# Performance work log

Hardware: AMD Instinct MI355X
Metric: run time of the kernel (lower is better)

## Reference

```python
import jax, jax.numpy as jnp
import numpy as np

EMBED_DIM = 1024
ZDIM = 128
STD = 0.02


def setup_inputs() -> dict:
    key = jax.random.key(0)
    ks = jax.random.split(key, 12)
    T, S, B, E, Z = 2048, 2048, 4, EMBED_DIM, ZDIM
    return {
        "query": jax.random.normal(ks[0], (T, B, E), jnp.float32),
        "key": jax.random.normal(ks[1], (S, B, E), jnp.float32),
        "Wq": jax.random.normal(ks[2], (2 * E + Z, E), jnp.float32) * STD,
        "bq": jnp.zeros((2 * E + Z,), jnp.float32),
        "Wk": jax.random.normal(ks[3], (Z, E), jnp.float32) * STD,
        "bk": jnp.zeros((Z,), jnp.float32),
        "Wv": jax.random.normal(ks[4], (E, E), jnp.float32) * STD,
        "bv": jnp.zeros((E,), jnp.float32),
        "Wh": jax.random.normal(ks[5], (E, E), jnp.float32) * STD,
        "bh": jnp.zeros((E,), jnp.float32),
        "gamma": jax.random.normal(ks[6], (2, Z), jnp.float32) * STD,
        "beta": jnp.zeros((2, Z), jnp.float32),
    }


def reference(query, key, Wq, bq, Wk, bk, Wv, bv, Wh, bh, gamma, beta):
    E, Z = EMBED_DIM, ZDIM
    scaling = Z ** (-0.5)
    # base: [T, B, 2E+Z]
    base = jnp.einsum('tbe,fe->tbf', query, Wq) + bq
    u = jax.nn.sigmoid(base[..., :E])                      # [T,B,E] output gate
    rq = jax.nn.silu(base[..., E:])                        # [T,B,E+Z]
    r = rq[..., :E]                                        # [T,B,E]
    q = rq[..., E:] * gamma[0] + beta[0]                   # [T,B,Z]
    k = jax.nn.silu(jnp.einsum('sbe,ze->sbz', key, Wk) + bk) * gamma[1] + beta[1]  # [S,B,Z]
    v = jax.nn.silu(jnp.einsum('sbe,fe->sbf', key, Wv) + bv)                       # [S,B,E]
    # softmax attention over context dim
    qk = jnp.einsum('tbz,sbz->bts', q * scaling, k)        # [B,T,S]
    attn = jax.nn.softmax(qk, axis=-1)
    h = jnp.einsum('bts,sbf->tbf', attn, v)                # [T,B,E]
    h = jnp.tanh(jnp.einsum('tbe,fe->tbf', h * r, Wh) + bh)
    out = query + u * (h - query)                          # addcmul
    return out
```

## Files before the change

### kernel.cpp

```cpp
#include <hip/hip_runtime.h>
#include <cstdint>
#include <cstddef>

using short8  = __attribute__((ext_vector_type(8))) short;
using floatx4 = __attribute__((ext_vector_type(4))) float;

#define DEV __device__ __forceinline__

DEV float u2f(unsigned short u){
  union { unsigned int i; float f; } c; c.i = ((unsigned int)u) << 16; return c.f;
}
DEV unsigned short f2u(float f){
  union { float f; unsigned int i; } c; c.f = f;
  unsigned int i = c.i;
  i += 0x7fffu + ((i >> 16) & 1u);
  return (unsigned short)(i >> 16);
}
DEV float sigmoidf_(float x){ return 1.0f / (1.0f + __expf(-x)); }
DEV float siluf_(float x){ return x / (1.0f + __expf(-x)); }

#define ASYNC_LD16(g, l) __builtin_amdgcn_global_load_lds( \
    (const __attribute__((address_space(1))) unsigned int*)(g), \
    (__attribute__((address_space(3))) unsigned int*)(l), 16, 0, 0)

#define MFMA_BF16 __builtin_amdgcn_mfma_f32_16x16x32_bf16

#define SBAR() asm volatile("s_barrier" ::: "memory")

constexpr float SCALING = 0.088388347648318447f;

__global__ __launch_bounds__(256) void cast_act(
    const float* __restrict__ q, const float* __restrict__ k,
    unsigned short* __restrict__ qo, unsigned short* __restrict__ ko)
{
  const int bid = blockIdx.x;
  const int e = threadIdx.x * 4;
  const float* src; unsigned short* dst;
  if (bid < 8192) {
    src = q + (long long)bid * 1024;
    dst = qo + (long long)bid * 1024;
  } else {
    const int m = bid - 8192;
    const int s = m >> 2, b = m & 3;
    src = k + (long long)m * 1024;
    dst = ko + ((long long)b * 2048 + s) * 1024;
  }
  const float4 v = *(const float4*)(src + e);
  ushort4 o; o.x=f2u(v.x); o.y=f2u(v.y); o.z=f2u(v.z); o.w=f2u(v.w);
  *(ushort4*)(dst + e) = o;
}

__global__ __launch_bounds__(256) void cast_w(
    const float* __restrict__ Wq, const float* __restrict__ Wk,
    const float* __restrict__ Wv, const float* __restrict__ Wh,
    unsigned short* __restrict__ oq, unsigned short* __restrict__ ok,
    unsigned short* __restrict__ ov, unsigned short* __restrict__ oh)
{
  const int bid = blockIdx.x;
  const int e = threadIdx.x * 4;
  const float* src; unsigned short* dst;
  if (bid < 2176)      { src = Wq + (long long)bid * 1024;        dst = oq + (long long)bid * 1024; }
  else if (bid < 2304) { src = Wk + (long long)(bid-2176) * 1024; dst = ok + (long long)(bid-2176) * 1024; }
  else if (bid < 3328) { src = Wv + (long long)(bid-2304) * 1024; dst = ov + (long long)(bid-2304) * 1024; }
  else                 { src = Wh + (long long)(bid-3328) * 1024; dst = oh + (long long)(bid-3328) * 1024; }
  const float4 v = *(const float4*)(src + e);
  ushort4 o; o.x=f2u(v.x); o.y=f2u(v.y); o.z=f2u(v.z); o.w=f2u(v.w);
  *(ushort4*)(dst + e) = o;
}

template<int EPI>
__global__ __launch_bounds__(256, 2)
void gemm_bt(const unsigned short* __restrict__ A, long long bsA, int lda,
             const unsigned short* __restrict__ Bm, long long bsB, int ldb,
             int K,
             const float* __restrict__ bias,
             const float* __restrict__ gam,
             const float* __restrict__ bet,
             float* __restrict__ f0,
             unsigned short* __restrict__ b0,
             unsigned short* __restrict__ b1,
             const unsigned short* __restrict__ rmul,
             const float* __restrict__ qin)
{
  __shared__ __align__(16) unsigned short As[128][64];
  __shared__ __align__(16) unsigned short Bs[128][64];

  const int tid = threadIdx.x;
  const int bm = blockIdx.x, bn = blockIdx.y, bz = blockIdx.z;
  const unsigned short* Ag = A  + (long long)bz * bsA;
  const unsigned short* Bg = Bm + (long long)bz * bsB;
  const int row0 = bm * 128;
  const int col0 = bn * 128;

  const int lane = tid & 63;
  const int wv   = tid >> 6;
  const int wm   = (wv & 1) * 64;
  const int wn   = (wv >> 1) * 64;
  const int lr   = lane & 15;
  const int lq   = lane >> 4;
  const int r7   = lr & 7;

  const unsigned short* gA[4]; const unsigned short* gB[4];
  unsigned short* lA[4]; unsigned short* lB[4];
  #pragma unroll
  for (int i = 0; i < 4; i++) {
    const int c  = tid + i * 256;
    const int rr = c >> 3;
    const int gc = (c & 7) ^ (rr & 7);
    gA[i] = Ag + (long long)(row0 + rr) * lda + gc * 8;
    gB[i] = Bg + (long long)(col0 + rr) * ldb + gc * 8;
    lA[i] = &As[0][0] + c * 8;
    lB[i] = &Bs[0][0] + c * 8;
  }

  floatx4 acc[4][4];
  const floatx4 zero = {0.f, 0.f, 0.f, 0.f};
  #pragma unroll
  for (int i = 0; i < 4; i++)
    #pragma unroll
    for (int j = 0; j < 4; j++) acc[i][j] = zero;

  for (int kt = 0; kt < K; kt += 64) {
    #pragma unroll
    for (int i = 0; i < 4; i++) {
      ASYNC_LD16(gA[i] + kt, lA[i]);
      ASYNC_LD16(gB[i] + kt, lB[i]);
    }
    __syncthreads();
    #pragma unroll
    for (int ks = 0; ks < 64; ks += 32) {
      const int k8 = ks >> 3;
      short8 af[4], bfv[4];
      #pragma unroll
      for (int i = 0; i < 4; i++) {
        const int sc = (lq + k8) ^ r7;
        af[i]  = *(const short8*)(&As[wm + i*16 + lr][sc * 8]);
        bfv[i] = *(const short8*)(&Bs[wn + i*16 + lr][sc * 8]);
      }
      #pragma unroll
      for (int mi = 0; mi < 4; mi++)
        #pragma unroll
        for (int ni = 0; ni < 4; ni++)
          acc[mi][ni] = MFMA_BF16(af[mi], bfv[ni], acc[mi][ni], 0, 0, 0);
    }
    __syncthreads();
  }

  #pragma unroll
  for (int mi = 0; mi < 4; mi++) {
    float s4[4];
    float iv[4];
    if constexpr (EPI == 3) {
      #pragma unroll
      for (int r = 0; r < 4; r++) s4[r] = 0.f;
    }
    if constexpr (EPI == 4) {
      #pragma unroll
      for (int r = 0; r < 4; r++) {
        const int gm = row0 + wm + mi * 16 + lq * 4 + r;
        iv[r] = 1.0f / f0[(long long)bz * 2048 + gm];
      }
    }
    #pragma unroll
    for (int ni = 0; ni < 4; ni++) {
      #pragma unroll
      for (int r = 0; r < 4; r++) {
        const int gm = row0 + wm + mi * 16 + lq * 4 + r;
        const int gn = col0 + wn + ni * 16 + lr;
        float v = acc[mi][ni][r];
        if constexpr (EPI == 2) {
          v += bias[gm];
          const int b = gn >> 11, s = gn & 2047;
          b0[((long long)b * 1024 + gm) * 2048 + s] = f2u(siluf_(v));
        } else if constexpr (EPI == 3) {
          const float e = __expf(v * SCALING);
          b0[(long long)bz * 2048 * 2048 + (long long)gm * 2048 + gn] = f2u(e);
          s4[r] += e;
        } else if constexpr (EPI == 4) {
          const long long idx = ((long long)gm * 4 + bz) * 1024 + gn;
          b0[idx] = f2u(v * iv[r] * u2f(rmul[idx]));
        } else {
          const long long idx = (long long)gm * 1024 + gn;
          const float tv = tanhf(v + bias[gn]);
          const float qv = qin[idx];
          f0[idx] = qv + u2f(rmul[idx]) * (tv - qv);
        }
      }
    }
    if constexpr (EPI == 3) {
      #pragma unroll
      for (int r = 0; r < 4; r++) {
        float s = s4[r];
        #pragma unroll
        for (int m2 = 8; m2 >= 1; m2 >>= 1) s += __shfl_xor(s, m2);
        if (lr == 0) {
          const int gm = row0 + wm + mi * 16 + lq * 4 + r;
          atomicAdd(f0 + (long long)bz * 2048 + gm, s);
        }
      }
    }
  }
}

__global__ __launch_bounds__(256, 2)
void gemm_nz128(const unsigned short* __restrict__ A0, const unsigned short* __restrict__ A1,
                const unsigned short* __restrict__ B0, const unsigned short* __restrict__ B1,
                const float* __restrict__ bi0, const float* __restrict__ bi1,
                const float* __restrict__ g0,  const float* __restrict__ g1,
                const float* __restrict__ be0, const float* __restrict__ be1,
                unsigned short* __restrict__ o0, unsigned short* __restrict__ o1)
{
  __shared__ __align__(16) unsigned short As[128][64];
  __shared__ __align__(16) unsigned short Bs[128][64];

  const int tid = threadIdx.x;
  const int bm = blockIdx.x;
  const int z  = blockIdx.z;
  const unsigned short* Ag = z ? A1 : A0;
  const unsigned short* Bg = z ? B1 : B0;
  const float* bias = z ? bi1 : bi0;
  const float* gam  = z ? g1  : g0;
  const float* bet  = z ? be1 : be0;
  unsigned short* ob = z ? o1 : o0;
  const int row0 = bm * 128;

  const int lane = tid & 63;
  const int wv   = tid >> 6;
  const int wm   = (wv & 1) * 64;
  const int wn   = (wv >> 1) * 64;
  const int lr   = lane & 15;
  const int lq   = lane >> 4;
  const int r7   = lr & 7;

  const unsigned short* gA[4]; const unsigned short* gB[4];
  unsigned short* lA[4]; unsigned short* lB[4];
  #pragma unroll
  for (int i = 0; i < 4; i++) {
    const int c  = tid + i * 256;
    const int rr = c >> 3;
    const int gc = (c & 7) ^ (rr & 7);
    gA[i] = Ag + (long long)(row0 + rr) * 1024 + gc * 8;
    gB[i] = Bg + (long long)rr * 1024 + gc * 8;
    lA[i] = &As[0][0] + c * 8;
    lB[i] = &Bs[0][0] + c * 8;
  }

  floatx4 acc[4][4];
  const floatx4 zero = {0.f, 0.f, 0.f, 0.f};
  #pragma unroll
  for (int i = 0; i < 4; i++)
    #pragma unroll
    for (int j = 0; j < 4; j++) acc[i][j] = zero;

  for (int kt = 0; kt < 1024; kt += 64) {
    #pragma unroll
    for (int i = 0; i < 4; i++) {
      ASYNC_LD16(gA[i] + kt, lA[i]);
      ASYNC_LD16(gB[i] + kt, lB[i]);
    }
    __syncthreads();
    #pragma unroll
    for (int ks = 0; ks < 64; ks += 32) {
      const int k8 = ks >> 3;
      short8 af[4], bfv[4];
      #pragma unroll
      for (int i = 0; i < 4; i++) {
        const int sc = (lq + k8) ^ r7;
        af[i]  = *(const short8*)(&As[wm + i*16 + lr][sc * 8]);
        bfv[i] = *(const short8*)(&Bs[wn + i*16 + lr][sc * 8]);
      }
      #pragma unroll
      for (int mi = 0; mi < 4; mi++)
        #pragma unroll
        for (int ni = 0; ni < 4; ni++)
          acc[mi][ni] = MFMA_BF16(af[mi], bfv[ni], acc[mi][ni], 0, 0, 0);
    }
    __syncthreads();
  }

  #pragma unroll
  for (int mi = 0; mi < 4; mi++)
    #pragma unroll
    for (int ni = 0; ni < 4; ni++)
      #pragma unroll
      for (int r = 0; r < 4; r++) {
        const int gm = row0 + wm + mi * 16 + lq * 4 + r;
        const int gn = wn + ni * 16 + lr;
        float v = acc[mi][ni][r] + bias[gn];
        ob[(long long)gm * 128 + gn] = f2u(siluf_(v) * gam[gn] + bet[gn]);
      }
}

__global__ __launch_bounds__(512, 2)
void gemm256(const unsigned short* __restrict__ A, int lda,
             const unsigned short* __restrict__ Bm, int ldb,
             int K,
             const float* __restrict__ bias,
             float* __restrict__ f0,
             unsigned short* __restrict__ b0)
{
  __shared__ __align__(16) unsigned short Ls[65536];

  const int tid = threadIdx.x;
  const int bm = blockIdx.x, bn = blockIdx.y;
  const int row0 = bm * 256;
  const int col0 = bn * 256;

  const int lane = tid & 63;
  const int wv   = tid >> 6;
  const int wr   = (wv >> 2) * 128;
  const int wc   = (wv & 3) * 64;
  const int lr   = lane & 15;
  const int lq   = lane >> 4;
  const int r7   = lr & 7;

  const int rr0 = tid >> 3;
  const int swz = ((tid & 7) ^ (rr0 & 7)) * 8;
  const unsigned short* gA0 = A  + (long long)(row0 + rr0) * lda + swz;
  const unsigned short* gB0 = Bm + (long long)(col0 + rr0) * ldb + swz;
  const long long sA64 = 64LL * lda, sB64 = 64LL * ldb;
  unsigned short* lA0 = &Ls[0]     + tid * 8;
  unsigned short* lB0 = &Ls[16384] + tid * 8;

  floatx4 acc[8][4];
  const floatx4 zero = {0.f, 0.f, 0.f, 0.f};
  #pragma unroll
  for (int i = 0; i < 8; i++)
    #pragma unroll
    for (int j = 0; j < 4; j++) acc[i][j] = zero;

  const int NT = K >> 6;

  #pragma unroll
  for (int i = 0; i < 4; i++) ASYNC_LD16(gA0 + i * sA64,      lA0 + i * 4096);
  #pragma unroll
  for (int i = 0; i < 4; i++) ASYNC_LD16(gB0 + i * sB64,      lB0 + i * 4096);
  #pragma unroll
  for (int i = 0; i < 4; i++) ASYNC_LD16(gA0 + i * sA64 + 64, lA0 + i * 4096 + 32768);
  #pragma unroll
  for (int i = 0; i < 4; i++) ASYNC_LD16(gB0 + i * sB64 + 64, lB0 + i * 4096 + 32768);
  asm volatile("s_waitcnt vmcnt(8)" ::: "memory");
  SBAR();

  for (int t = 0; t < NT; ++t) {
    const int cb = (t & 1) << 15;
    const unsigned short* Ab = &Ls[cb];
    const unsigned short* Bb = &Ls[cb + 16384];
    const bool st = (t + 2) < NT;
    const int kt2 = (t + 2) << 6;

    short8 afA[4][2], afB[4][2], bf01[2][2], bf23[2][2];

    #pragma unroll
    for (int mi = 0; mi < 4; mi++)
      #pragma unroll
      for (int k = 0; k < 2; k++)
        afA[mi][k] = *(const short8*)(Ab + (wr + mi*16 + lr) * 64 + (((k<<2) + lq) ^ r7) * 8);
    #pragma unroll
    for (int ni = 0; ni < 2; ni++)
      #pragma unroll
      for (int k = 0; k < 2; k++)
        bf01[ni][k] = *(const short8*)(Bb + (wc + ni*16 + lr) * 64 + (((k<<2) + lq) ^ r7) * 8);
    asm volatile("s_waitcnt lgkmcnt(8)" ::: "memory");
    SBAR();
    asm volatile("s_waitcnt lgkmcnt(0)" ::: "memory");
    __builtin_amdgcn_sched_barrier(0);
    __builtin_amdgcn_s_setprio(1);
    #pragma unroll
    for (int mi = 0; mi < 4; mi++)
      #pragma unroll
      for (int ni = 0; ni < 2; ni++)
        #pragma unroll
        for (int k = 0; k < 2; k++)
          acc[mi][ni] = MFMA_BF16(afA[mi][k], bf01[ni][k], acc[mi][ni], 0, 0, 0);
    __builtin_amdgcn_s_setprio(0);
    SBAR();

    #pragma unroll
    for (int ni = 0; ni < 2; ni++)
      #pragma unroll
      for (int k = 0; k < 2; k++)
        bf23[ni][k] = *(const short8*)(Bb + (wc + (ni+2)*16 + lr) * 64 + (((k<<2) + lq) ^ r7) * 8);
    SBAR();
    asm volatile("s_waitcnt lgkmcnt(0)" ::: "memory");
    __builtin_amdgcn_sched_barrier(0);
    __builtin_amdgcn_s_setprio(1);
    #pragma unroll
    for (int mi = 0; mi < 4; mi++)
      #pragma unroll
      for (int ni = 0; ni < 2; ni++)
        #pragma unroll
        for (int k = 0; k < 2; k++)
          acc[mi][ni+2] = MFMA_BF16(afA[mi][k], bf23[ni][k], acc[mi][ni+2], 0, 0, 0);
    __builtin_amdgcn_s_setprio(0);
    SBAR();

    #pragma unroll
    for (int mi = 0; mi < 4; mi++)
      #pragma unroll
      for (int k = 0; k < 2; k++)
        afB[mi][k] = *(const short8*)(Ab + (wr + (mi+4)*16 + lr) * 64 + (((k<<2) + lq) ^ r7) * 8);
    if (st) {
      #pragma unroll
      for (int i = 0; i < 4; i++) ASYNC_LD16(gB0 + i * sB64 + kt2, lB0 + i * 4096 + cb);
    }
    SBAR();
    asm volatile("s_waitcnt lgkmcnt(0)" ::: "memory");
    __builtin_amdgcn_sched_barrier(0);
    __builtin_amdgcn_s_setprio(1);
    #pragma unroll
    for (int mi = 0; mi < 4; mi++)
      #pragma unroll
      for (int ni = 0; ni < 2; ni++)
        #pragma unroll
        for (int k = 0; k < 2; k++)
          acc[mi+4][ni] = MFMA_BF16(afB[mi][k], bf01[ni][k], acc[mi+4][ni], 0, 0, 0);
    __builtin_amdgcn_s_setprio(0);
    SBAR();

    if (st) {
      #pragma unroll
      for (int i = 0; i < 4; i++) ASYNC_LD16(gA0 + i * sA64 + kt2, lA0 + i * 4096 + cb);
    }
    SBAR();
    __builtin_amdgcn_s_setprio(1);
    #pragma unroll
    for (int mi = 0; mi < 4; mi++)
      #pragma unroll
      for (int ni = 0; ni < 2; ni++)
        #pragma unroll
        for (int k = 0; k < 2; k++)
          acc[mi+4][ni+2] = MFMA_BF16(afB[mi][k], bf23[ni][k], acc[mi+4][ni+2], 0, 0, 0);
    __builtin_amdgcn_s_setprio(0);
    if (st) { asm volatile("s_waitcnt vmcnt(8)" ::: "memory"); }
    else    { asm volatile("s_waitcnt vmcnt(0)" ::: "memory"); }
    SBAR();
  }

  #pragma unroll
  for (int mi = 0; mi < 8; mi++)
    #pragma unroll
    for (int ni = 0; ni < 4; ni++)
      #pragma unroll
      for (int r = 0; r < 4; r++) {
        const int gm = row0 + wr + mi * 16 + lq * 4 + r;
        const int gn = col0 + wc + ni * 16 + lr;
        float v = acc[mi][ni][r] + bias[gn];
        if (gn < 1024) {
          ((unsigned short*)f0)[(long long)gm * 1024 + gn] = f2u(sigmoidf_(v));
        } else {
          b0[(long long)gm * 1024 + (gn - 1024)] = f2u(siluf_(v));
        }
      }
}

extern "C" void kernel_launch(void* const* d_in, const int* in_sizes, int n_in,
                              void* d_out, int out_size, void* d_ws, size_t ws_size,
                              hipStream_t stream)
{
  (void)in_sizes; (void)n_in; (void)out_size; (void)ws_size;
  const float* query = (const float*)d_in[0];
  const float* key   = (const float*)d_in[1];
  const float* Wq    = (const float*)d_in[2];
  const float* bq    = (const float*)d_in[3];
  const float* Wk    = (const float*)d_in[4];
  const float* bk    = (const float*)d_in[5];
  const float* Wv    = (const float*)d_in[6];
  const float* bv    = (const float*)d_in[7];
  const float* Wh    = (const float*)d_in[8];
  const float* bh    = (const float*)d_in[9];
  const float* gamma = (const float*)d_in[10];
  const float* beta  = (const float*)d_in[11];
  float* out = (float*)d_out;

  char* p = (char*)d_ws;
  auto take = [&](size_t bytes) -> char* {
    char* r = p; p += (bytes + 255) & ~(size_t)255; return r;
  };
  unsigned short* qbf = (unsigned short*)take(8192ULL * 1024 * 2);
  unsigned short* kbr = (unsigned short*)take(8192ULL * 1024 * 2);
  unsigned short* Wqb = (unsigned short*)take(2176ULL * 1024 * 2);
  unsigned short* Wkb = (unsigned short*)take(128ULL  * 1024 * 2);
  unsigned short* Wvb = (unsigned short*)take(1024ULL * 1024 * 2);
  unsigned short* Whb = (unsigned short*)take(1024ULL * 1024 * 2);
  unsigned short* ub  = (unsigned short*)take(8192ULL * 1024 * 2);
  unsigned short* rbf = (unsigned short*)take(8192ULL * 1024 * 2);
  unsigned short* qpj = (unsigned short*)take(8192ULL * 128 * 2);
  unsigned short* kpj = (unsigned short*)take(8192ULL * 128 * 2);
  unsigned short* vT  = (unsigned short*)take(4ULL * 1024 * 2048 * 2);
  unsigned short* Pb  = (unsigned short*)take(4ULL * 2048 * 2048 * 2);
  unsigned short* hrb = (unsigned short*)take(8192ULL * 1024 * 2);
  float*          rs  = (float*)take(4ULL * 2048 * 4);

  dim3 blk(256);
  dim3 gblk(512);
  cast_act<<<16384, blk, 0, stream>>>(query, key, qbf, kbr);
  cast_w<<<4352, blk, 0, stream>>>(Wq, Wk, Wv, Wh, Wqb, Wkb, Wvb, Whb);
  hipMemsetAsync(rs, 0, 4ULL * 2048 * 4, stream);

  gemm_nz128<<<dim3(64, 1, 2), blk, 0, stream>>>(
      qbf, kbr, Wqb + 2048LL * 1024, Wkb,
      bq + 2048, bk, gamma, gamma + 128, beta, beta + 128, qpj, kpj);
  gemm256<<<dim3(32, 8, 1), gblk, 0, stream>>>(qbf, 1024, Wqb, 1024, 1024,
      bq, (float*)ub, rbf);
  gemm_bt<2><<<dim3(8, 64, 1), blk, 0, stream>>>(Wvb, 0, 1024, kbr, 0, 1024, 1024,
      bv, nullptr, nullptr, nullptr, vT, nullptr, nullptr, nullptr);
  gemm_bt<3><<<dim3(16, 16, 4), blk, 0, stream>>>(qpj, 128, 512, kpj, 2048LL * 128, 128, 128,
      nullptr, nullptr, nullptr, rs, Pb, nullptr, nullptr, nullptr);
  gemm_bt<4><<<dim3(16, 8, 4), blk, 0, stream>>>(Pb, 2048LL * 2048, 2048,
      vT, 1024LL * 2048, 2048, 2048,
      nullptr, nullptr, nullptr, rs, hrb, nullptr, rbf, nullptr);
  gemm_bt<5><<<dim3(64, 8, 1), blk, 0, stream>>>(hrb, 0, 1024, Whb, 0, 1024, 1024,
      bh, nullptr, nullptr, out, nullptr, nullptr, ub, query);
}
```

Measured before the change: 351.8 us.

## Move V-projection, PV and output GEMMs to 256x128 double-buffered async-LDS kernel

Adds a new 512-thread GEMM kernel with 256x128 tiles, double-buffered direct-to-LDS async loads and split MFMA phases. The V projection, attention-times-V and output projection GEMMs now use it instead of the 128x128 synchronous gemm_bt, which is cut down to only the softmax-numerator epilogue. It also removes several workgroup barriers from the gemm256 main loop. The larger tiles aim for better operand reuse and for overlapping loads with compute, at the cost of more LDS per block and fewer blocks. Dropping the barriers risks LDS races in gemm256.

```diff
diff --git a/kernel.cpp b/kernel.cpp
--- a/kernel.cpp
+++ b/kernel.cpp
@@ -73,14 +73,8 @@
 void gemm_bt(const unsigned short* __restrict__ A, long long bsA, int lda,
              const unsigned short* __restrict__ Bm, long long bsB, int ldb,
              int K,
-             const float* __restrict__ bias,
-             const float* __restrict__ gam,
-             const float* __restrict__ bet,
              float* __restrict__ f0,
-             unsigned short* __restrict__ b0,
-             unsigned short* __restrict__ b1,
-             const unsigned short* __restrict__ rmul,
-             const float* __restrict__ qin)
+             unsigned short* __restrict__ b0)
 {
   __shared__ __align__(16) unsigned short As[128][64];
   __shared__ __align__(16) unsigned short Bs[128][64];
@@ -149,54 +143,27 @@
   #pragma unroll
   for (int mi = 0; mi < 4; mi++) {
     float s4[4];
-    float iv[4];
-    if constexpr (EPI == 3) {
-      #pragma unroll
-      for (int r = 0; r < 4; r++) s4[r] = 0.f;
-    }
-    if constexpr (EPI == 4) {
-      #pragma unroll
-      for (int r = 0; r < 4; r++) {
-        const int gm = row0 + wm + mi * 16 + lq * 4 + r;
-        iv[r] = 1.0f / f0[(long long)bz * 2048 + gm];
-      }
-    }
+    #pragma unroll
+    for (int r = 0; r < 4; r++) s4[r] = 0.f;
     #pragma unroll
     for (int ni = 0; ni < 4; ni++) {
       #pragma unroll
       for (int r = 0; r < 4; r++) {
         const int gm = row0 + wm + mi * 16 + lq * 4 + r;
         const int gn = col0 + wn + ni * 16 + lr;
-        float v = acc[mi][ni][r];
-        if constexpr (EPI == 2) {
-          v += bias[gm];
-          const int b = gn >> 11, s = gn & 2047;
-          b0[((long long)b * 1024 + gm) * 2048 + s] = f2u(siluf_(v));
-        } else if constexpr (EPI == 3) {
-          const float e = __expf(v * SCALING);
-          b0[(long long)bz * 2048 * 2048 + (long long)gm * 2048 + gn] = f2u(e);
-          s4[r] += e;
-        } else if constexpr (EPI == 4) {
-          const long long idx = ((long long)gm * 4 + bz) * 1024 + gn;
-          b0[idx] = f2u(v * iv[r] * u2f(rmul[idx]));
-        } else {
-          const long long idx = (long long)gm * 1024 + gn;
-          const float tv = tanhf(v + bias[gn]);
-          const float qv = qin[idx];
-          f0[idx] = qv + u2f(rmul[idx]) * (tv - qv);
-        }
-      }
-    }
-    if constexpr (EPI == 3) {
-      #pragma unroll
-      for (int r = 0; r < 4; r++) {
-        float s = s4[r];
-        #pragma unroll
-        for (int m2 = 8; m2 >= 1; m2 >>= 1) s += __shfl_xor(s, m2);
-        if (lr == 0) {
-          const int gm = row0 + wm + mi * 16 + lq * 4 + r;
-          atomicAdd(f0 + (long long)bz * 2048 + gm, s);
-        }
+        const float e = __expf(acc[mi][ni][r] * SCALING);
+        b0[(long long)bz * 2048 * 2048 + (long long)gm * 2048 + gn] = f2u(e);
+        s4[r] += e;
+      }
+    }
+    #pragma unroll
+    for (int r = 0; r < 4; r++) {
+      float s = s4[r];
+      #pragma unroll
+      for (int m2 = 8; m2 >= 1; m2 >>= 1) s += __shfl_xor(s, m2);
+      if (lr == 0) {
+        const int gm = row0 + wm + mi * 16 + lq * 4 + r;
+        atomicAdd(f0 + (long long)bz * 2048 + gm, s);
       }
     }
   }
@@ -361,8 +328,6 @@
       #pragma unroll
       for (int k = 0; k < 2; k++)
         bf01[ni][k] = *(const short8*)(Bb + (wc + ni*16 + lr) * 64 + (((k<<2) + lq) ^ r7) * 8);
-    asm volatile("s_waitcnt lgkmcnt(8)" ::: "memory");
-    SBAR();
     asm volatile("s_waitcnt lgkmcnt(0)" ::: "memory");
     __builtin_amdgcn_sched_barrier(0);
     __builtin_amdgcn_s_setprio(1);
@@ -381,7 +346,6 @@
       #pragma unroll
       for (int k = 0; k < 2; k++)
         bf23[ni][k] = *(const short8*)(Bb + (wc + (ni+2)*16 + lr) * 64 + (((k<<2) + lq) ^ r7) * 8);
-    SBAR();
     asm volatile("s_waitcnt lgkmcnt(0)" ::: "memory");
     __builtin_amdgcn_sched_barrier(0);
     __builtin_amdgcn_s_setprio(1);
@@ -404,7 +368,6 @@
       #pragma unroll
       for (int i = 0; i < 4; i++) ASYNC_LD16(gB0 + i * sB64 + kt2, lB0 + i * 4096 + cb);
     }
-    SBAR();
     asm volatile("s_waitcnt lgkmcnt(0)" ::: "memory");
     __builtin_amdgcn_sched_barrier(0);
     __builtin_amdgcn_s_setprio(1);
@@ -422,7 +385,6 @@
       #pragma unroll
       for (int i = 0; i < 4; i++) ASYNC_LD16(gA0 + i * sA64 + kt2, lA0 + i * 4096 + cb);
     }
-    SBAR();
     __builtin_amdgcn_s_setprio(1);
     #pragma unroll
     for (int mi = 0; mi < 4; mi++)
@@ -452,6 +414,149 @@
           b0[(long long)gm * 1024 + (gn - 1024)] = f2u(siluf_(v));
         }
       }
+}
+
+template<int EPI>
+__global__ __launch_bounds__(512, 2)
+void gemm_n128(const unsigned short* __restrict__ A, long long bsA, int lda,
+               const unsigned short* __restrict__ Bm, long long bsB, int ldb,
+               int K,
+               const float* __restrict__ bias,
+               float* __restrict__ f0,
+               unsigned short* __restrict__ b0,
+               const unsigned short* __restrict__ rmul,
+               const float* __restrict__ qin)
+{
+  __shared__ __align__(16) unsigned short Ls[49152];
+
+  const int tid = threadIdx.x;
+  const int bm = blockIdx.x, bn = blockIdx.y, bz = blockIdx.z;
+  const unsigned short* Ag = A  + (long long)bz * bsA;
+  const unsigned short* Bg = Bm + (long long)bz * bsB;
+  const int row0 = bm * 256;
+  const int col0 = bn * 128;
+
+  const int lane = tid & 63;
+  const int wv   = tid >> 6;
+  const int wr   = (wv & 3) * 64;
+  const int wc   = (wv >> 2) * 64;
+  const int lr   = lane & 15;
+  const int lq   = lane >> 4;
+  const int r7   = lr & 7;
+
+  const int rr0 = tid >> 3;
+  const int swz = ((tid & 7) ^ (rr0 & 7)) * 8;
+  const unsigned short* gA0 = Ag + (long long)(row0 + rr0) * lda + swz;
+  const unsigned short* gB0 = Bg + (long long)(col0 + rr0) * ldb + swz;
+  const long long sA64 = 64LL * lda, sB64 = 64LL * ldb;
+  unsigned short* lA0 = &Ls[0]     + tid * 8;
+  unsigned short* lB0 = &Ls[16384] + tid * 8;
+
+  floatx4 acc[4][4];
+  const floatx4 zero = {0.f, 0.f, 0.f, 0.f};
+  #pragma unroll
+  for (int i = 0; i < 4; i++)
+    #pragma unroll
+    for (int j = 0; j < 4; j++) acc[i][j] = zero;
+
+  const int NT = K >> 6;
+
+  #pragma unroll
+  for (int i = 0; i < 4; i++) ASYNC_LD16(gA0 + i * sA64,      lA0 + i * 4096);
+  #pragma unroll
+  for (int i = 0; i < 2; i++) ASYNC_LD16(gB0 + i * sB64,      lB0 + i * 4096);
+  #pragma unroll
+  for (int i = 0; i < 4; i++) ASYNC_LD16(gA0 + i * sA64 + 64, lA0 + i * 4096 + 24576);
+  #pragma unroll
+  for (int i = 0; i < 2; i++) ASYNC_LD16(gB0 + i * sB64 + 64, lB0 + i * 4096 + 24576);
+  asm volatile("s_waitcnt vmcnt(6)" ::: "memory");
+  SBAR();
+
+  for (int t = 0; t < NT; ++t) {
+    const int cb = (t & 1) * 24576;
+    const unsigned short* Ab = &Ls[cb];
+    const unsigned short* Bb = &Ls[cb + 16384];
+    const bool st = (t + 2) < NT;
+    const int kt2 = (t + 2) << 6;
+
+    short8 afA[4][2], bfv[4][2];
+
+    #pragma unroll
+    for (int mi = 0; mi < 4; mi++)
+      #pragma unroll
+      for (int k = 0; k < 2; k++)
+        afA[mi][k] = *(const short8*)(Ab + (wr + mi*16 + lr) * 64 + (((k<<2) + lq) ^ r7) * 8);
+    #pragma unroll
+    for (int ni = 0; ni < 4; ni++)
+      #pragma unroll
+      for (int k = 0; k < 2; k++)
+        bfv[ni][k] = *(const short8*)(Bb + (wc + ni*16 + lr) * 64 + (((k<<2) + lq) ^ r7) * 8);
+    asm volatile("s_waitcnt lgkmcnt(0)" ::: "memory");
+    __builtin_amdgcn_sched_barrier(0);
+    __builtin_amdgcn_s_setprio(1);
+    #pragma unroll
+    for (int mi = 0; mi < 4; mi++)
+      #pragma unroll
+      for (int ni = 0; ni < 2; ni++)
+        #pragma unroll
+        for (int k = 0; k < 2; k++)
+          acc[mi][ni] = MFMA_BF16(afA[mi][k], bfv[ni][k], acc[mi][ni], 0, 0, 0);
+    __builtin_amdgcn_s_setprio(0);
+    SBAR();
+
+    if (st) {
+      #pragma unroll
+      for (int i = 0; i < 4; i++) ASYNC_LD16(gA0 + i * sA64 + kt2, lA0 + i * 4096 + cb);
+      #pragma unroll
+      for (int i = 0; i < 2; i++) ASYNC_LD16(gB0 + i * sB64 + kt2, lB0 + i * 4096 + cb);
+    }
+    __builtin_amdgcn_s_setprio(1);
+    #pragma unroll
+    for (int mi = 0; mi < 4; mi++)
+      #pragma unroll
+      for (int ni = 0; ni < 2; ni++)
+        #pragma unroll
+        for (int k = 0; k < 2; k++)
+          acc[mi][ni+2] = MFMA_BF16(afA[mi][k], bfv[ni+2][k], acc[mi][ni+2], 0, 0, 0);
+    __builtin_amdgcn_s_setprio(0);
+    if (st) { asm volatile("s_waitcnt vmcnt(6)" ::: "memory"); }
+    else    { asm volatile("s_waitcnt vmcnt(0)" ::: "memory"); }
+    SBAR();
+  }
+
+  #pragma unroll
+  for (int mi = 0; mi < 4; mi++) {
+    float iv[4];
+    if constexpr (EPI == 4) {
+      #pragma unroll
+      for (int r = 0; r < 4; r++) {
+        const int gm = row0 + wr + mi * 16 + lq * 4 + r;
+        iv[r] = 1.0f / f0[(long long)bz * 2048 + gm];
+      }
+    }
+    #pragma unroll
+    for (int ni = 0; ni < 4; ni++) {
+      #pragma unroll
+      for (int r = 0; r < 4; r++) {
+        const int gm = row0 + wr + mi * 16 + lq * 4 + r;
+        const int gn = col0 + wc + ni * 16 + lr;
+        float v = acc[mi][ni][r];
+        if constexpr (EPI == 2) {
+          v += bias[gm];
+          const int b = gn >> 11, s = gn & 2047;
+          b0[((long long)b * 1024 + gm) * 2048 + s] = f2u(siluf_(v));
+        } else if constexpr (EPI == 4) {
+          const long long idx = ((long long)gm * 4 + bz) * 1024 + gn;
+          b0[idx] = f2u(v * iv[r] * u2f(rmul[idx]));
+        } else {
+          const long long idx = (long long)gm * 1024 + gn;
+          const float tv = tanhf(v + bias[gn]);
+          const float qv = qin[idx];
+          f0[idx] = qv + u2f(rmul[idx]) * (tv - qv);
+        }
+      }
+    }
+  }
 }
 
 extern "C" void kernel_launch(void* const* d_in, const int* in_sizes, int n_in,
@@ -503,13 +608,13 @@
       bq + 2048, bk, gamma, gamma + 128, beta, beta + 128, qpj, kpj);
   gemm256<<<dim3(32, 8, 1), gblk, 0, stream>>>(qbf, 1024, Wqb, 1024, 1024,
       bq, (float*)ub, rbf);
-  gemm_bt<2><<<dim3(8, 64, 1), blk, 0, stream>>>(Wvb, 0, 1024, kbr, 0, 1024, 1024,
-      bv, nullptr, nullptr, nullptr, vT, nullptr, nullptr, nullptr);
+  gemm_n128<2><<<dim3(4, 64, 1), gblk, 0, stream>>>(Wvb, 0, 1024, kbr, 0, 1024, 1024,
+      bv, nullptr, vT, nullptr, nullptr);
   gemm_bt<3><<<dim3(16, 16, 4), blk, 0, stream>>>(qpj, 128, 512, kpj, 2048LL * 128, 128, 128,
-      nullptr, nullptr, nullptr, rs, Pb, nullptr, nullptr, nullptr);
-  gemm_bt<4><<<dim3(16, 8, 4), blk, 0, stream>>>(Pb, 2048LL * 2048, 2048,
+      rs, Pb);
+  gemm_n128<4><<<dim3(8, 8, 4), gblk, 0, stream>>>(Pb, 2048LL * 2048, 2048,
       vT, 1024LL * 2048, 2048, 2048,
-      nullptr, nullptr, nullptr, rs, hrb, nullptr, rbf, nullptr);
-  gemm_bt<5><<<dim3(64, 8, 1), blk, 0, stream>>>(hrb, 0, 1024, Whb, 0, 1024, 1024,
-      bh, nullptr, nullptr, out, nullptr, nullptr, ub, query);
-}
+      nullptr, rs, hrb, rbf, nullptr);
+  gemm_n128<5><<<dim3(32, 8, 1), gblk, 0, stream>>>(hrb, 0, 1024, Whb, 0, 1024, 1024,
+      bh, out, nullptr, ub, query);
+}
```

Measured after the change: 342.2 us. 1.03x faster.
